# Kernel optimization log

Hardware: AMD Instinct MI355X
Metric: run time of the kernel (lower is better)

## Reference

```python
import jax, jax.numpy as jnp
import numpy as np

PH, PW = 7, 7  # pool_height, pool_width


def _bin_ids(n, lo, hi, d, nbins):
    """Assign each coordinate in [0,n) to its ROI bin (or to the dump segment `nbins`).

    Bins replicate the TF code: bin k covers [lo+k*d, lo+(k+1)*d) for k < nbins-1,
    and the last bin covers [lo+(nbins-1)*d, hi). d == (hi-lo)//nbins (trunc div).
    """
    coords = jnp.arange(n, dtype=jnp.int32)
    inside = (coords >= lo) & (coords < hi)
    b = jnp.minimum((coords - lo) // jnp.maximum(d, 1), nbins - 1)
    b = jnp.where(d > 0, b, nbins - 1)  # degenerate d==0: only last bin is non-empty
    return jnp.where(inside, b, nbins).astype(jnp.int32)


def _one_roi(image, roi, ph, pw):
    # image: [X, Y, C]; roi = (minX, minY, maxX, maxY) int32
    X, Y, C = image.shape
    minX, minY, maxX, maxY = roi[0], roi[1], roi[2], roi[3]
    dx = (maxX - minX) // pw
    dy = (maxY - minY) // ph
    xb = _bin_ids(X, minX, maxX, dx, pw)   # [X]
    yb = _bin_ids(Y, minY, maxY, dy, ph)   # [Y]
    # max over x within each x-bin -> [pw, Y, C]  (dump segment pw dropped)
    px = jax.ops.segment_max(image, xb, num_segments=pw + 1)[:pw]
    # max over y within each y-bin -> [ph, pw, C]
    py = jax.ops.segment_max(jnp.swapaxes(px, 0, 1), yb, num_segments=ph + 1)[:ph]
    return py  # [ph, pw, C], rows indexed by h (y-bins), cols by w (x-bins)


def setup_inputs() -> dict:
    key = jax.random.key(0)
    kf, kx1, kw, ky1, kh = jax.random.split(key, 5)
    B, H, W, C, N = 8, 128, 128, 128, 128
    features = jax.random.normal(kf, (B, H, W, C), dtype=jnp.float32)
    # valid ROIs: min < max, side length >= 2*pool so every bin is non-empty
    x1 = jax.random.randint(kx1, (B, N), 0, H // 2)
    wdt = jax.random.randint(kw, (B, N), 2 * PW, H // 2)
    y1 = jax.random.randint(ky1, (B, N), 0, W // 2)
    hgt = jax.random.randint(kh, (B, N), 2 * PH, W // 2)
    rois = jnp.stack([x1, y1, x1 + wdt, y1 + hgt], axis=-1).astype(jnp.int32)
    return {"features": features, "rois": rois}


def reference(features, rois):
    # features: [B, X, Y, C], rois: [B, N, 4] -> [B, N, PH, PW, C]
    per_img = jax.vmap(lambda img, r: _one_roi(img, r, PH, PW), in_axes=(None, 0))
    return jax.vmap(per_img)(features, rois)
```

## Files before the change

kernel.cpp:

```cpp
#include <hip/hip_runtime.h>

#define PH 7
#define PW 7

__global__ __launch_bounds__(64) void roi_maxpool_kernel(
    const float* __restrict__ feat,
    const int*   __restrict__ rois,
    float*       __restrict__ out,
    int X, int Y, int C, int N)
{
    const int hw = blockIdx.x;
    const int w  = hw % PW;
    const int h  = hw / PW;
    const int n  = blockIdx.y;
    const int b  = blockIdx.z;

    const int4 roi = *reinterpret_cast<const int4*>(&rois[(b * N + n) * 4]);
    const int minX = roi.x, minY = roi.y, maxX = roi.z, maxY = roi.w;

    const int dx = (maxX - minX) / PW;
    const int dy = (maxY - minY) / PH;

    const int xs = minX + w * dx;
    const int xe = (w == PW - 1) ? maxX : (xs + dx);
    const int ys = minY + h * dy;
    const int ye = (h == PH - 1) ? maxY : (ys + dy);

    const int t = threadIdx.x;
    const int c0 = 2 * t;

    float mx = -INFINITY;
    float my = -INFINITY;

    const int baseb = b * X * Y * C;
    for (int x = xs; x < xe; ++x) {
        const char* rowp = (const char*)(feat + baseb + x * Y * C + ys * C + c0);
        const int stride = C * (int)sizeof(float);
        #pragma unroll 4
        for (int y = ys; y < ye; ++y) {
            float2 v = *reinterpret_cast<const float2*>(rowp);
            rowp += stride;
            mx = fmaxf(mx, v.x);
            my = fmaxf(my, v.y);
        }
    }

    const int oidx = (((b * N + n) * PH + h) * PW + w) * C + c0;
    float2 r; r.x = mx; r.y = my;
    *reinterpret_cast<float2*>(&out[oidx]) = r;
}

extern "C" void kernel_launch(void* const* d_in, const int* in_sizes, int n_in,
                              void* d_out, int out_size, void* d_ws, size_t ws_size,
                              hipStream_t stream) {
    const float* feat = (const float*)d_in[0];
    const int*   rois = (const int*)d_in[1];
    float*       out  = (float*)d_out;

    const int B = 8, X = 128, Y = 128, C = 128;
    const int N = in_sizes[1] / (4 * B);

    dim3 grid(PH * PW, N, B);
    roi_maxpool_kernel<<<grid, 64, 0, stream>>>(feat, rois, out, X, Y, C, N);
}
```

Measured before the change: 155.1 us.

## Use float4 loads with two-row split, 4-wave blocks, and XCD-aware block swizzle

Measured after the change: 158.5 us. +2.2%, slower.

```diff
diff --git a/kernel.cpp b/kernel.cpp
--- a/kernel.cpp
+++ b/kernel.cpp
@@ -2,18 +2,35 @@
 
 #define PH 7
 #define PW 7
+#define BINS   (PH * PW)
+#define CHUNKS ((BINS + 3) / 4)
 
-__global__ __launch_bounds__(64) void roi_maxpool_kernel(
+__global__ __launch_bounds__(256) void roi_maxpool_kernel(
     const float* __restrict__ feat,
     const int*   __restrict__ rois,
     float*       __restrict__ out,
-    int X, int Y, int C, int N)
+    int X, int Y, int C, int N, int B, int xcd_swizzle)
 {
-    const int hw = blockIdx.x;
-    const int w  = hw % PW;
-    const int h  = hw / PW;
-    const int n  = blockIdx.y;
-    const int b  = blockIdx.z;
+    int b, n, xc;
+    if (xcd_swizzle) {
+        const int id = blockIdx.x;
+        b  = id & 7;
+        const int k = id >> 3;
+        n  = k / CHUNKS;
+        xc = k % CHUNKS;
+    } else {
+        const int id = blockIdx.x;
+        xc = id % CHUNKS;
+        const int k = id / CHUNKS;
+        n  = k % N;
+        b  = k / N;
+    }
+
+    const int wv = threadIdx.x >> 6;
+    const int hw = xc * 4 + wv;
+    if (hw >= BINS) return;
+    const int w = hw % PW;
+    const int h = hw / PW;
 
     const int4 roi = *reinterpret_cast<const int4*>(&rois[(b * N + n) * 4]);
     const int minX = roi.x, minY = roi.y, maxX = roi.z, maxY = roi.w;
@@ -26,28 +43,34 @@
     const int ys = minY + h * dy;
     const int ye = (h == PH - 1) ? maxY : (ys + dy);
 
-    const int t = threadIdx.x;
-    const int c0 = 2 * t;
+    const int t  = threadIdx.x & 63;
+    const int pp = t >> 5;
+    const int c0 = (t & 31) * 4;
 
-    float mx = -INFINITY;
-    float my = -INFINITY;
+    float4 m; m.x = m.y = m.z = m.w = -INFINITY;
 
-    const int baseb = b * X * Y * C;
+    const long stride = 2L * C * sizeof(float);
     for (int x = xs; x < xe; ++x) {
-        const char* rowp = (const char*)(feat + baseb + x * Y * C + ys * C + c0);
-        const int stride = C * (int)sizeof(float);
-        #pragma unroll 4
-        for (int y = ys; y < ye; ++y) {
-            float2 v = *reinterpret_cast<const float2*>(rowp);
-            rowp += stride;
-            mx = fmaxf(mx, v.x);
-            my = fmaxf(my, v.y);
+        const char* p = (const char*)(feat + ((long)(b * X + x) * Y + ys + pp) * C + c0);
+        for (int y = ys + pp; y < ye; y += 2) {
+            float4 v = *reinterpret_cast<const float4*>(p);
+            p += stride;
+            m.x = fmaxf(m.x, v.x);
+            m.y = fmaxf(m.y, v.y);
+            m.z = fmaxf(m.z, v.z);
+            m.w = fmaxf(m.w, v.w);
         }
     }
 
-    const int oidx = (((b * N + n) * PH + h) * PW + w) * C + c0;
-    float2 r; r.x = mx; r.y = my;
-    *reinterpret_cast<float2*>(&out[oidx]) = r;
+    m.x = fmaxf(m.x, __shfl_xor(m.x, 32));
+    m.y = fmaxf(m.y, __shfl_xor(m.y, 32));
+    m.z = fmaxf(m.z, __shfl_xor(m.z, 32));
+    m.w = fmaxf(m.w, __shfl_xor(m.w, 32));
+
+    if (t < 32) {
+        const int oidx = (((b * N + n) * PH + h) * PW + w) * C + c0;
+        *reinterpret_cast<float4*>(&out[oidx]) = m;
+    }
 }
 
 extern "C" void kernel_launch(void* const* d_in, const int* in_sizes, int n_in,
@@ -57,9 +80,11 @@
     const int*   rois = (const int*)d_in[1];
     float*       out  = (float*)d_out;
 
-    const int B = 8, X = 128, Y = 128, C = 128;
+    const int X = 128, Y = 128, C = 128;
+    const int B = in_sizes[0] / (X * Y * C);
     const int N = in_sizes[1] / (4 * B);
 
-    dim3 grid(PH * PW, N, B);
-    roi_maxpool_kernel<<<grid, 64, 0, stream>>>(feat, rois, out, X, Y, C, N);
+    const int swz = (B == 8) ? 1 : 0;
+    dim3 grid(B * N * CHUNKS);
+    roi_maxpool_kernel<<<grid, 256, 0, stream>>>(feat, rois, out, X, Y, C, N, B, swz);
 }
```

## Swizzle blocks by image across XCDs and use float4 loads with split-row unroll

Applied to the files above, without the earlier changes.

After: 139.0 us. 1.12x faster.

```diff
diff --git a/kernel.cpp b/kernel.cpp
--- a/kernel.cpp
+++ b/kernel.cpp
@@ -2,18 +2,22 @@
 
 #define PH 7
 #define PW 7
+#define BINS (PH * PW)
 
 __global__ __launch_bounds__(64) void roi_maxpool_kernel(
     const float* __restrict__ feat,
     const int*   __restrict__ rois,
     float*       __restrict__ out,
-    int X, int Y, int C, int N)
+    int X, int Y, int C, int N, int xcd_swizzle)
 {
-    const int hw = blockIdx.x;
+    const int id = blockIdx.x;
+    int b, rest;
+    if (xcd_swizzle) { b = id & 7; rest = id >> 3; }
+    else             { b = id / (N * BINS); rest = id % (N * BINS); }
+    const int n  = rest / BINS;
+    const int hw = rest % BINS;
     const int w  = hw % PW;
     const int h  = hw / PW;
-    const int n  = blockIdx.y;
-    const int b  = blockIdx.z;
 
     const int4 roi = *reinterpret_cast<const int4*>(&rois[(b * N + n) * 4]);
     const int minX = roi.x, minY = roi.y, maxX = roi.z, maxY = roi.w;
@@ -26,28 +30,46 @@
     const int ys = minY + h * dy;
     const int ye = (h == PH - 1) ? maxY : (ys + dy);
 
-    const int t = threadIdx.x;
-    const int c0 = 2 * t;
+    const int t  = threadIdx.x;
+    const int pp = t >> 5;
+    const int c0 = (t & 31) * 4;
 
-    float mx = -INFINITY;
-    float my = -INFINITY;
+    const int y0    = ys + pp;
+    const int cntL  = (ye - y0 + 1) >> 1;
+    const int ylast = y0 + 2 * (cntL - 1);
+    const int cnt0  = (ye - ys + 1) >> 1;
 
-    const int baseb = b * X * Y * C;
-    for (int x = xs; x < xe; ++x) {
-        const char* rowp = (const char*)(feat + baseb + x * Y * C + ys * C + c0);
-        const int stride = C * (int)sizeof(float);
-        #pragma unroll 4
-        for (int y = ys; y < ye; ++y) {
-            float2 v = *reinterpret_cast<const float2*>(rowp);
-            rowp += stride;
-            mx = fmaxf(mx, v.x);
-            my = fmaxf(my, v.y);
+    float4 m; m.x = m.y = m.z = m.w = -INFINITY;
+
+    for (int xi = xs; xi < xe; xi += 2) {
+        const int x1 = (xi + 1 < xe) ? (xi + 1) : (xe - 1);
+        const float* r0 = feat + ((long)(b * X + xi) * Y) * C + c0;
+        const float* r1 = feat + ((long)(b * X + x1) * Y) * C + c0;
+        for (int j = 0; j < cnt0; j += 2) {
+            int ya = y0 + 2 * j;
+            int yb = ya + 2;
+            ya = (ya < ylast) ? ya : ylast;
+            yb = (yb < ylast) ? yb : ylast;
+            const float4 v0 = *reinterpret_cast<const float4*>(r0 + (long)ya * C);
+            const float4 v1 = *reinterpret_cast<const float4*>(r0 + (long)yb * C);
+            const float4 v2 = *reinterpret_cast<const float4*>(r1 + (long)ya * C);
+            const float4 v3 = *reinterpret_cast<const float4*>(r1 + (long)yb * C);
+            m.x = fmaxf(fmaxf(m.x, fmaxf(v0.x, v1.x)), fmaxf(v2.x, v3.x));
+            m.y = fmaxf(fmaxf(m.y, fmaxf(v0.y, v1.y)), fmaxf(v2.y, v3.y));
+            m.z = fmaxf(fmaxf(m.z, fmaxf(v0.z, v1.z)), fmaxf(v2.z, v3.z));
+            m.w = fmaxf(fmaxf(m.w, fmaxf(v0.w, v1.w)), fmaxf(v2.w, v3.w));
         }
     }
 
-    const int oidx = (((b * N + n) * PH + h) * PW + w) * C + c0;
-    float2 r; r.x = mx; r.y = my;
-    *reinterpret_cast<float2*>(&out[oidx]) = r;
+    m.x = fmaxf(m.x, __shfl_xor(m.x, 32));
+    m.y = fmaxf(m.y, __shfl_xor(m.y, 32));
+    m.z = fmaxf(m.z, __shfl_xor(m.z, 32));
+    m.w = fmaxf(m.w, __shfl_xor(m.w, 32));
+
+    if (t < 32) {
+        const int oidx = (((b * N + n) * PH + h) * PW + w) * C + c0;
+        *reinterpret_cast<float4*>(&out[oidx]) = m;
+    }
 }
 
 extern "C" void kernel_launch(void* const* d_in, const int* in_sizes, int n_in,
@@ -57,9 +79,11 @@
     const int*   rois = (const int*)d_in[1];
     float*       out  = (float*)d_out;
 
-    const int B = 8, X = 128, Y = 128, C = 128;
+    const int X = 128, Y = 128, C = 128;
+    const int B = in_sizes[0] / (X * Y * C);
     const int N = in_sizes[1] / (4 * B);
 
-    dim3 grid(PH * PW, N, B);
-    roi_maxpool_kernel<<<grid, 64, 0, stream>>>(feat, rois, out, X, Y, C, N);
+    const int swz = (B == 8) ? 1 : 0;
+    dim3 grid(B * N * BINS);
+    roi_maxpool_kernel<<<grid, 64, 0, stream>>>(feat, rois, out, X, Y, C, N, swz);
 }
```

## Restructure ROI pooling to one block per ROI with column-strip waves

Applied to the files above, without the earlier changes.

Result: slower. 158.4 us (+2.1%).

```diff
diff --git a/kernel.cpp b/kernel.cpp
--- a/kernel.cpp
+++ b/kernel.cpp
@@ -3,51 +3,103 @@
 #define PH 7
 #define PW 7
 
-__global__ __launch_bounds__(64) void roi_maxpool_kernel(
+__device__ __forceinline__ float4 max4(float4 a, float4 b) {
+    float4 r;
+    r.x = fmaxf(a.x, b.x); r.y = fmaxf(a.y, b.y);
+    r.z = fmaxf(a.z, b.z); r.w = fmaxf(a.w, b.w);
+    return r;
+}
+
+__global__ __launch_bounds__(512, 8) void roi_maxpool_kernel(
     const float* __restrict__ feat,
     const int*   __restrict__ rois,
     float*       __restrict__ out,
-    int X, int Y, int C, int N)
+    int N, int xcd_swizzle)
 {
-    const int hw = blockIdx.x;
-    const int w  = hw % PW;
-    const int h  = hw / PW;
-    const int n  = blockIdx.y;
-    const int b  = blockIdx.z;
+    const int X = 128, Y = 128, C = 128;
+
+    const int id = blockIdx.x;
+    int b, n;
+    if (xcd_swizzle) { b = id & 7; n = id >> 3; }
+    else             { b = id / N; n = id % N; }
+
+    const int wv = threadIdx.x >> 6;
+    const int t  = threadIdx.x & 63;
+    const int px = t >> 5;
+    const int c0 = (t & 31) * 4;
 
     const int4 roi = *reinterpret_cast<const int4*>(&rois[(b * N + n) * 4]);
     const int minX = roi.x, minY = roi.y, maxX = roi.z, maxY = roi.w;
-
     const int dx = (maxX - minX) / PW;
     const int dy = (maxY - minY) / PH;
 
-    const int xs = minX + w * dx;
-    const int xe = (w == PW - 1) ? maxX : (xs + dx);
-    const int ys = minY + h * dy;
-    const int ye = (h == PH - 1) ? maxY : (ys + dy);
+    int xs, xe, w;
+    if (wv < 6) {
+        w = wv; xs = minX + wv * dx; xe = xs + dx;
+    } else {
+        w = 6;
+        const int s6  = minX + 6 * dx;
+        const int mid = s6 + ((maxX - s6 + 1) >> 1);
+        xs = (wv == 6) ? s6 : mid;
+        xe = (wv == 6) ? mid : maxX;
+    }
 
-    const int t = threadIdx.x;
-    const int c0 = 2 * t;
+    float4 acc[PH];
+    #pragma unroll
+    for (int h = 0; h < PH; ++h) { acc[h].x = acc[h].y = acc[h].z = acc[h].w = -INFINITY; }
 
-    float mx = -INFINITY;
-    float my = -INFINITY;
-
-    const int baseb = b * X * Y * C;
-    for (int x = xs; x < xe; ++x) {
-        const char* rowp = (const char*)(feat + baseb + x * Y * C + ys * C + c0);
-        const int stride = C * (int)sizeof(float);
-        #pragma unroll 4
-        for (int y = ys; y < ye; ++y) {
-            float2 v = *reinterpret_cast<const float2*>(rowp);
-            rowp += stride;
-            mx = fmaxf(mx, v.x);
-            my = fmaxf(my, v.y);
+    const float* base = feat + (long)b * X * Y * C + c0;
+    for (int xi = xs; xi < xe; xi += 2) {
+        int xl = xi + px; xl = (xl < xe) ? xl : (xe - 1);
+        const float* p = base + (xl * Y + minY) * C;
+        int ysh = minY;
+        #pragma unroll
+        for (int h = 0; h < PH; ++h) {
+            const int yeh = (h == PH - 1) ? maxY : (ysh + dy);
+            int cnt = yeh - ysh;
+            while (cnt >= 2) {
+                const float4 v0 = *reinterpret_cast<const float4*>(p);
+                const float4 v1 = *reinterpret_cast<const float4*>(p + C);
+                p += 2 * C; cnt -= 2;
+                acc[h] = max4(acc[h], max4(v0, v1));
+            }
+            if (cnt) {
+                const float4 v0 = *reinterpret_cast<const float4*>(p);
+                p += C;
+                acc[h] = max4(acc[h], v0);
+            }
+            ysh = yeh;
         }
     }
 
-    const int oidx = (((b * N + n) * PH + h) * PW + w) * C + c0;
-    float2 r; r.x = mx; r.y = my;
-    *reinterpret_cast<float2*>(&out[oidx]) = r;
+    #pragma unroll
+    for (int h = 0; h < PH; ++h) {
+        acc[h].x = fmaxf(acc[h].x, __shfl_xor(acc[h].x, 32));
+        acc[h].y = fmaxf(acc[h].y, __shfl_xor(acc[h].y, 32));
+        acc[h].z = fmaxf(acc[h].z, __shfl_xor(acc[h].z, 32));
+        acc[h].w = fmaxf(acc[h].w, __shfl_xor(acc[h].w, 32));
+    }
+
+    __shared__ float lds[PH * 128];
+    if (wv == 7 && t < 32) {
+        #pragma unroll
+        for (int h = 0; h < PH; ++h)
+            *reinterpret_cast<float4*>(&lds[h * 128 + c0]) = acc[h];
+    }
+    __syncthreads();
+
+    if (t < 32 && wv <= 6) {
+        if (wv == 6) {
+            #pragma unroll
+            for (int h = 0; h < PH; ++h)
+                acc[h] = max4(acc[h], *reinterpret_cast<const float4*>(&lds[h * 128 + c0]));
+        }
+        #pragma unroll
+        for (int h = 0; h < PH; ++h) {
+            const long o = ((((long)b * N + n) * PH + h) * PW + w) * C + c0;
+            *reinterpret_cast<float4*>(&out[o]) = acc[h];
+        }
+    }
 }
 
 extern "C" void kernel_launch(void* const* d_in, const int* in_sizes, int n_in,
@@ -57,9 +109,11 @@
     const int*   rois = (const int*)d_in[1];
     float*       out  = (float*)d_out;
 
-    const int B = 8, X = 128, Y = 128, C = 128;
+    const int X = 128, Y = 128, C = 128;
+    const int B = in_sizes[0] / (X * Y * C);
     const int N = in_sizes[1] / (4 * B);
 
-    dim3 grid(PH * PW, N, B);
-    roi_maxpool_kernel<<<grid, 64, 0, stream>>>(feat, rois, out, X, Y, C, N);
+    const int swz = (B == 8) ? 1 : 0;
+    dim3 grid(B * N);
+    roi_maxpool_kernel<<<grid, 512, 0, stream>>>(feat, rois, out, N, swz);
 }
```
